# Kernel tuning notes

Hardware: AMD Instinct MI355X
Metric: run time of the kernel (lower is better)

## Reference

```python
import jax, jax.numpy as jnp
from jax import lax
import numpy as np

B, S, R, V, C = 64, 512, 64, 30522, 2


def setup_inputs() -> dict:
    key = jax.random.key(0)
    k1, k2, k3, k4 = jax.random.split(key, 4)
    input_ids = jax.random.randint(k1, (B, S), 0, V, dtype=jnp.int32)
    mask = jnp.ones((B, S), dtype=jnp.int32)
    segment_ids = jnp.zeros((B, S), dtype=jnp.int32)
    seq_lengths = jnp.full((B,), S, dtype=jnp.int32)
    # scale 1/sqrt(R) keeps the 512-step matrix chain numerically stable in fp32
    G_weight = jax.random.normal(k2, (V, R * R), dtype=jnp.float32) * (1.0 / float(np.sqrt(R)))
    G1_weight = jax.random.normal(k3, (R, 1), dtype=jnp.float32) * 0.1
    lin_W = jax.random.normal(k4, (C, R), dtype=jnp.float32) * 0.1
    lin_b = jnp.zeros((C,), dtype=jnp.float32)
    return {"input_ids": input_ids, "mask": mask, "segment_ids": segment_ids,
            "seq_lengths": seq_lengths, "G_weight": G_weight, "G1_weight": G1_weight,
            "lin_W": lin_W, "lin_b": lin_b}


def reference(input_ids, mask, segment_ids, seq_lengths, G_weight, G1_weight, lin_W, lin_b):
    b, s = input_ids.shape
    r = lin_W.shape[1]
    # embedding lookup -> per-token r x r matrices: (b, s, r, r)
    encoded = jnp.take(G_weight, input_ids, axis=0).reshape(b, s, r, r)
    # initial state: G1.weight.view(-1, r) repeated over batch -> (b, 1, r)
    init = jnp.broadcast_to(G1_weight.reshape(1, 1, r), (b, 1, r)).astype(G_weight.dtype)
    # sequential matrix-chain recurrence over sequence positions
    xs = jnp.moveaxis(encoded, 1, 0)  # (s, b, r, r)

    def step(carry, M):
        return jnp.einsum('bij,bjk->bik', carry, M), None

    result, _ = lax.scan(step, init, xs)  # (b, 1, r)
    # torch F.normalize(dim=2): x / max(||x||_2, eps)
    norm = jnp.sqrt(jnp.sum(result * result, axis=2, keepdims=True))
    normed = result / jnp.maximum(norm, 1e-12)
    encoded_x = jnp.squeeze(normed, axis=1)  # (b, r)
    out = encoded_x @ lin_W.T + lin_b  # (b, n_class)
    return jnp.squeeze(out)
```

## Files before the change

kernel.cpp:

```cpp
#include <hip/hip_runtime.h>
#include <math.h>

#define SEQ   512
#define RDIM  64
#define NB    64
#define SEGL  16
#define SEGS  32

typedef short  v4s __attribute__((ext_vector_type(4)));
typedef float  v4f __attribute__((ext_vector_type(4)));
typedef unsigned int u32x2 __attribute__((ext_vector_type(2)));

__device__ __forceinline__ v4f mfma16(v4s a, v4s b, v4f c) {
#if __has_builtin(__builtin_amdgcn_mfma_f32_16x16x16bf16_1k)
    return __builtin_amdgcn_mfma_f32_16x16x16bf16_1k(a, b, c, 0, 0, 0);
#else
    v4f d;
    asm volatile("v_mfma_f32_16x16x16_bf16 %0, %1, %2, %3"
                 : "=v"(d) : "v"(a), "v"(b), "v"(c));
    return d;
#endif
}

__device__ __forceinline__ unsigned short bf16_rne(float x) {
    unsigned int u = __float_as_uint(x);
    unsigned int r = u + 0x7FFFu + ((u >> 16) & 1u);
    return (unsigned short)(r >> 16);
}
__device__ __forceinline__ float bf16_tof(unsigned short h) {
    return __uint_as_float(((unsigned int)h) << 16);
}

__global__ __launch_bounds__(64, 2)
void seg_kernel(const int* __restrict__ input_ids,
                const float* __restrict__ G_weight,
                float* __restrict__ ws)
{
    const int lane = threadIdx.x & 63;
    const int g    = lane >> 4;
    const int rl   = lane & 15;
    const int blk  = blockIdx.x;
    const int idb  = blk << 4;

    v4f acc[4][4];
#pragma unroll
    for (int m = 0; m < 4; ++m)
#pragma unroll
        for (int jb = 0; jb < 4; ++jb)
#pragma unroll
            for (int r = 0; r < 4; ++r)
                acc[m][jb][r] = (m == jb && rl == ((g << 2) + r)) ? 1.0f : 0.0f;

    float4 pa[16];
    {
        const int id0 = __builtin_amdgcn_readfirstlane(input_ids[idb + 15]);
        const float* bp = G_weight + (((size_t)id0) << 12);
#pragma unroll
        for (int m = 0; m < 4; ++m) {
            const float* gp = bp + (((m << 4) + rl) << 6) + (g << 2);
#pragma unroll
            for (int kc = 0; kc < 4; ++kc)
                pa[(m << 2) + kc] = *(const float4*)(gp + (kc << 4));
        }
    }

    int pend = input_ids[idb + 14];

#pragma unroll 1
    for (int i = 0; i < 16; ++i) {
        v4s Bh[4][4], Bl[4][4];
#pragma unroll
        for (int kc = 0; kc < 4; ++kc)
#pragma unroll
            for (int jb = 0; jb < 4; ++jb) {
                v4s h, l;
#pragma unroll
                for (int r = 0; r < 4; ++r) {
                    const float x = acc[kc][jb][r];
                    const unsigned short hh = bf16_rne(x);
                    h[r] = (short)hh;
                    l[r] = (short)bf16_rne(x - bf16_tof(hh));
                }
                Bh[kc][jb] = h;
                Bl[kc][jb] = l;
            }

        const int idn = __builtin_amdgcn_readfirstlane(pend);

#pragma unroll
        for (int m = 0; m < 4; ++m) {
            v4s Ah[4], Al[4];
#pragma unroll
            for (int kc = 0; kc < 4; ++kc) {
                const float4 x = pa[(m << 2) + kc];
                const float e[4] = {x.x, x.y, x.z, x.w};
#pragma unroll
                for (int j = 0; j < 4; ++j) {
                    const unsigned short hh = bf16_rne(e[j]);
                    Ah[kc][j] = (short)hh;
                    Al[kc][j] = (short)bf16_rne(e[j] - bf16_tof(hh));
                }
            }
            if (i < 15) {
                const float* gp = G_weight + (((size_t)idn) << 12)
                                + (((m << 4) + rl) << 6) + (g << 2);
#pragma unroll
                for (int kc = 0; kc < 4; ++kc)
                    pa[(m << 2) + kc] = *(const float4*)(gp + (kc << 4));
            }
#pragma unroll
            for (int jb = 0; jb < 4; ++jb) {
                v4f d = {0.f, 0.f, 0.f, 0.f};
#pragma unroll
                for (int kc = 0; kc < 4; ++kc) {
                    d = mfma16(Ah[kc], Bh[kc][jb], d);
                    d = mfma16(Al[kc], Bh[kc][jb], d);
                    d = mfma16(Ah[kc], Bl[kc][jb], d);
                }
                acc[m][jb] = d;
            }
        }

        {
            int nx = 13 - i;
            nx = (nx < 0) ? 0 : nx;
            pend = input_ids[idb + nx];
        }
    }

    float* wp = ws + (((size_t)blk) << 12);
#pragma unroll
    for (int m = 0; m < 4; ++m)
#pragma unroll
        for (int jb = 0; jb < 4; ++jb)
#pragma unroll
            for (int r = 0; r < 4; ++r)
                wp[(((m << 4) + (g << 2) + r) << 6) + (jb << 4) + rl] = acc[m][jb][r];
}

__device__ __forceinline__ float qreduce4(float x) {
#if __has_builtin(__builtin_amdgcn_permlane16_swap) && __has_builtin(__builtin_amdgcn_permlane32_swap)
    u32x2 a = __builtin_amdgcn_permlane16_swap(__float_as_uint(x), __float_as_uint(x), false, false);
    const float y = __uint_as_float(a.x) + __uint_as_float(a.y);
    u32x2 c = __builtin_amdgcn_permlane32_swap(__float_as_uint(y), __float_as_uint(y), false, false);
    return __uint_as_float(c.x) + __uint_as_float(c.y);
#else
    x += __shfl_xor(x, 16, 64);
    x += __shfl_xor(x, 32, 64);
    return x;
#endif
}

#define STRD 12

__global__ __launch_bounds__(512, 2)
void chain2_kernel(const float* __restrict__ ws,
                   const float* __restrict__ G1_weight,
                   const float* __restrict__ lin_W,
                   const float* __restrict__ lin_b,
                   float* __restrict__ out)
{
    __shared__ __align__(16) float part[2][RDIM][STRD];

    const int tid  = threadIdx.x;
    const int lane = tid & 63;
    const int w    = tid >> 6;
    const int b    = blockIdx.x;
    const int sub  = lane >> 4;
    const int p16  = lane & 15;

    const int k0 = (w << 3) + sub;
    float vm0 = G1_weight[k0];
    float vm1 = G1_weight[k0 + 4];

    const size_t lo0 = (size_t)((w << 9) + (sub << 6) + (p16 << 2));
    const size_t lo1 = lo0 + 256;

    float4 bufA[16], bufB[16];

#define ISSUE2(S, T) do {                                                  \
        const float* bp_ = ws + (((size_t)((b << 5) + (T))) << 12);        \
        bufA[S] = *(const float4*)(bp_ + lo0);                             \
        bufB[S] = *(const float4*)(bp_ + lo1);                             \
    } while (0)

#pragma unroll
    for (int p = 0; p < 16; ++p) ISSUE2(p, p);

#define BODY2(S, T) do {                                                       \
        const float4 a_ = bufA[S];                                             \
        const float4 c_ = bufB[S];                                             \
        float fx = fmaf(vm0, a_.x, vm1 * c_.x);                                \
        float fy = fmaf(vm0, a_.y, vm1 * c_.y);                                \
        float fz = fmaf(vm0, a_.z, vm1 * c_.z);                                \
        float fw = fmaf(vm0, a_.w, vm1 * c_.w);                                \
        { int nx_ = (T) + 16; nx_ = (nx_ < SEGS) ? nx_ : (SEGS - 1);           \
          ISSUE2(S, nx_); }                                                    \
        fx = qreduce4(fx); fy = qreduce4(fy);                                  \
        fz = qreduce4(fz); fw = qreduce4(fw);                                  \
        const float wv_ = (sub == 0) ? fx : (sub == 1) ? fy                    \
                        : (sub == 2) ? fz : fw;                                \
        part[(T) & 1][(p16 << 2) + sub][w] = wv_;                              \
        asm volatile("s_waitcnt lgkmcnt(0)\n\ts_barrier" ::: "memory");        \
        {                                                                      \
            const float4* pk0_ = (const float4*)&part[(T) & 1][k0][0];         \
            const float4  r0_  = pk0_[0], r1_ = pk0_[1];                       \
            vm0 = ((r0_.x + r0_.y) + (r0_.z + r0_.w))                          \
                + ((r1_.x + r1_.y) + (r1_.z + r1_.w));                         \
            const float4* pk1_ = (const float4*)&part[(T) & 1][k0 + 4][0];     \
            const float4  s0_  = pk1_[0], s1_ = pk1_[1];                       \
            vm1 = ((s0_.x + s0_.y) + (s0_.z + s0_.w))                          \
                + ((s1_.x + s1_.y) + (s1_.z + s1_.w));                         \
        }                                                                      \
    } while (0)

    BODY2( 0,  0); BODY2( 1,  1); BODY2( 2,  2); BODY2( 3,  3);
    BODY2( 4,  4); BODY2( 5,  5); BODY2( 6,  6); BODY2( 7,  7);
    BODY2( 8,  8); BODY2( 9,  9); BODY2(10, 10); BODY2(11, 11);
    BODY2(12, 12); BODY2(13, 13); BODY2(14, 14); BODY2(15, 15);
    BODY2( 0, 16); BODY2( 1, 17); BODY2( 2, 18); BODY2( 3, 19);
    BODY2( 4, 20); BODY2( 5, 21); BODY2( 6, 22); BODY2( 7, 23);
    BODY2( 8, 24); BODY2( 9, 25); BODY2(10, 26); BODY2(11, 27);
    BODY2(12, 28); BODY2(13, 29); BODY2(14, 30); BODY2(15, 31);

    asm volatile("s_waitcnt vmcnt(0)" ::: "memory");

    float vj;
    {
        const float4* pj = (const float4*)&part[1][lane][0];
        const float4 q0 = pj[0], q1 = pj[1];
        vj = ((q0.x + q0.y) + (q0.z + q0.w)) + ((q1.x + q1.y) + (q1.z + q1.w));
    }

    if (w == 0) {
        float ss = vj * vj;
#pragma unroll
        for (int off = 32; off >= 1; off >>= 1)
            ss += __shfl_xor(ss, off, 64);
        const float inv = 1.0f / fmaxf(sqrtf(ss), 1e-12f);
        const float nj  = vj * inv;

        float d0 = nj * lin_W[lane];
        float d1 = nj * lin_W[RDIM + lane];
#pragma unroll
        for (int off = 32; off >= 1; off >>= 1) {
            d0 += __shfl_xor(d0, off, 64);
            d1 += __shfl_xor(d1, off, 64);
        }
        if (lane == 0) {
            out[b * 2 + 0] = d0 + lin_b[0];
            out[b * 2 + 1] = d1 + lin_b[1];
        }
    }
}

__global__ __launch_bounds__(512, 2)
void matchain_kernel(const int* __restrict__ input_ids,
                     const float* __restrict__ G_weight,
                     const float* __restrict__ G1_weight,
                     const float* __restrict__ lin_W,
                     const float* __restrict__ lin_b,
                     float* __restrict__ out)
{
    __shared__ int   ids[SEQ];
    __shared__ __align__(16) float part[2][RDIM][STRD];

    const int tid  = threadIdx.x;
    const int lane = tid & 63;
    const int w    = tid >> 6;
    const int b    = blockIdx.x;
    const int sub  = lane >> 4;
    const int p16  = lane & 15;

    ids[tid] = input_ids[b * SEQ + tid];
    __syncthreads();

    const int k0 = (w << 3) + sub;
    float vm0 = G1_weight[k0];
    float vm1 = G1_weight[k0 + 4];

    const size_t lo0 = (size_t)((w << 9) + (sub << 6) + (p16 << 2));
    const size_t lo1 = lo0 + 256;

    float4 bufA[16], bufB[16];

#define ISSUE(S, id_) do {                                        \
        const float* bp_ = G_weight + (((size_t)(id_)) << 12);    \
        bufA[S] = *(const float4*)(bp_ + lo0);                    \
        bufB[S] = *(const float4*)(bp_ + lo1);                    \
    } while (0)

#pragma unroll
    for (int p = 0; p < 16; ++p)
        ISSUE(p, __builtin_amdgcn_readfirstlane(ids[p]));

    int pend = ids[16];

#define BODY(S, K) do {                                                        \
        const float4 a_ = bufA[S];                                             \
        const float4 c_ = bufB[S];                                             \
        float fx = fmaf(vm0, a_.x, vm1 * c_.x);                                \
        float fy = fmaf(vm0, a_.y, vm1 * c_.y);                                \
        float fz = fmaf(vm0, a_.z, vm1 * c_.z);                                \
        float fw = fmaf(vm0, a_.w, vm1 * c_.w);                                \
        {                                                                      \
            const int idn_ = __builtin_amdgcn_readfirstlane(pend);             \
            ISSUE(S, idn_);                                                    \
            int nx_ = t0 + (K) + 17;                                           \
            nx_ = (nx_ < SEQ) ? nx_ : (SEQ - 1);                               \
            pend = ids[nx_];                                                   \
        }                                                                      \
        fx = qreduce4(fx); fy = qreduce4(fy);                                  \
        fz = qreduce4(fz); fw = qreduce4(fw);                                  \
        const float wv_ = (sub == 0) ? fx : (sub == 1) ? fy                    \
                        : (sub == 2) ? fz : fw;                                \
        part[(K) & 1][(p16 << 2) + sub][w] = wv_;                              \
        asm volatile("s_waitcnt lgkmcnt(0)\n\ts_barrier" ::: "memory");        \
        {                                                                      \
            const float4* pk0_ = (const float4*)&part[(K) & 1][k0][0];         \
            const float4  r0_  = pk0_[0], r1_ = pk0_[1];                       \
            vm0 = ((r0_.x + r0_.y) + (r0_.z + r0_.w))                          \
                + ((r1_.x + r1_.y) + (r1_.z + r1_.w));                         \
            const float4* pk1_ = (const float4*)&part[(K) & 1][k0 + 4][0];     \
            const float4  s0_  = pk1_[0], s1_ = pk1_[1];                       \
            vm1 = ((s0_.x + s0_.y) + (s0_.z + s0_.w))                          \
                + ((s1_.x + s1_.y) + (s1_.z + s1_.w));                         \
        }                                                                      \
    } while (0)

#pragma unroll 1
    for (int t0 = 0; t0 < SEQ; t0 += 16) {
        BODY( 0,  0); BODY( 1,  1); BODY( 2,  2); BODY( 3,  3);
        BODY( 4,  4); BODY( 5,  5); BODY( 6,  6); BODY( 7,  7);
        BODY( 8,  8); BODY( 9,  9); BODY(10, 10); BODY(11, 11);
        BODY(12, 12); BODY(13, 13); BODY(14, 14); BODY(15, 15);
    }

    asm volatile("s_waitcnt vmcnt(0)" ::: "memory");

    float vj;
    {
        const float4* pj = (const float4*)&part[1][lane][0];
        const float4 q0 = pj[0], q1 = pj[1];
        vj = ((q0.x + q0.y) + (q0.z + q0.w)) + ((q1.x + q1.y) + (q1.z + q1.w));
    }

    if (w == 0) {
        float ss = vj * vj;
#pragma unroll
        for (int off = 32; off >= 1; off >>= 1)
            ss += __shfl_xor(ss, off, 64);
        const float inv = 1.0f / fmaxf(sqrtf(ss), 1e-12f);
        const float nj  = vj * inv;

        float d0 = nj * lin_W[lane];
        float d1 = nj * lin_W[RDIM + lane];
#pragma unroll
        for (int off = 32; off >= 1; off >>= 1) {
            d0 += __shfl_xor(d0, off, 64);
            d1 += __shfl_xor(d1, off, 64);
        }
        if (lane == 0) {
            out[b * 2 + 0] = d0 + lin_b[0];
            out[b * 2 + 1] = d1 + lin_b[1];
        }
    }
}

extern "C" void kernel_launch(void* const* d_in, const int* in_sizes, int n_in,
                              void* d_out, int out_size, void* d_ws, size_t ws_size,
                              hipStream_t stream) {
    const int*   input_ids = (const int*)d_in[0];
    const float* G_weight  = (const float*)d_in[4];
    const float* G1_weight = (const float*)d_in[5];
    const float* lin_W     = (const float*)d_in[6];
    const float* lin_b     = (const float*)d_in[7];
    float*       out       = (float*)d_out;

    const size_t need = (size_t)NB * SEGS * RDIM * RDIM * sizeof(float);
    if (ws_size >= need) {
        float* ws = (float*)d_ws;
        seg_kernel<<<NB * SEGS, 64, 0, stream>>>(input_ids, G_weight, ws);
        chain2_kernel<<<NB, 512, 0, stream>>>(ws, G1_weight, lin_W, lin_b, out);
    } else {
        matchain_kernel<<<NB, 512, 0, stream>>>(input_ids, G_weight, G1_weight,
                                                lin_W, lin_b, out);
    }
}
```

Baseline: 125.0 us.

## Fuse segment-product and chain kernels with per-batch atomic counters

Merges the segment matrix-product kernel and the chain/output kernel into a single launch. Each 512-thread block runs eight segment waves, then signals a per-batch counter with a release atomic. The first 64 blocks spin until all 32 segments of their batch are done and then run the chain reduction. This removes the second kernel launch and the gap between kernels, but adds a memset, spin-waiting, and a dependence on the first 64 blocks being co-resident with producer blocks to avoid deadlock.

```diff
diff --git a/kernel.cpp b/kernel.cpp
--- a/kernel.cpp
+++ b/kernel.cpp
@@ -4,8 +4,10 @@
 #define SEQ   512
 #define RDIM  64
 #define NB    64
-#define SEGL  16
 #define SEGS  32
+#define NSEG  2048
+#define STRD  12
+#define WS_MATS_BYTES ((size_t)NSEG * RDIM * RDIM * sizeof(float))
 
 typedef short  v4s __attribute__((ext_vector_type(4)));
 typedef float  v4f __attribute__((ext_vector_type(4)));
@@ -29,113 +31,6 @@
 }
 __device__ __forceinline__ float bf16_tof(unsigned short h) {
     return __uint_as_float(((unsigned int)h) << 16);
-}
-
-__global__ __launch_bounds__(64, 2)
-void seg_kernel(const int* __restrict__ input_ids,
-                const float* __restrict__ G_weight,
-                float* __restrict__ ws)
-{
-    const int lane = threadIdx.x & 63;
-    const int g    = lane >> 4;
-    const int rl   = lane & 15;
-    const int blk  = blockIdx.x;
-    const int idb  = blk << 4;
-
-    v4f acc[4][4];
-#pragma unroll
-    for (int m = 0; m < 4; ++m)
-#pragma unroll
-        for (int jb = 0; jb < 4; ++jb)
-#pragma unroll
-            for (int r = 0; r < 4; ++r)
-                acc[m][jb][r] = (m == jb && rl == ((g << 2) + r)) ? 1.0f : 0.0f;
-
-    float4 pa[16];
-    {
-        const int id0 = __builtin_amdgcn_readfirstlane(input_ids[idb + 15]);
-        const float* bp = G_weight + (((size_t)id0) << 12);
-#pragma unroll
-        for (int m = 0; m < 4; ++m) {
-            const float* gp = bp + (((m << 4) + rl) << 6) + (g << 2);
-#pragma unroll
-            for (int kc = 0; kc < 4; ++kc)
-                pa[(m << 2) + kc] = *(const float4*)(gp + (kc << 4));
-        }
-    }
-
-    int pend = input_ids[idb + 14];
-
-#pragma unroll 1
-    for (int i = 0; i < 16; ++i) {
-        v4s Bh[4][4], Bl[4][4];
-#pragma unroll
-        for (int kc = 0; kc < 4; ++kc)
-#pragma unroll
-            for (int jb = 0; jb < 4; ++jb) {
-                v4s h, l;
-#pragma unroll
-                for (int r = 0; r < 4; ++r) {
-                    const float x = acc[kc][jb][r];
-                    const unsigned short hh = bf16_rne(x);
-                    h[r] = (short)hh;
-                    l[r] = (short)bf16_rne(x - bf16_tof(hh));
-                }
-                Bh[kc][jb] = h;
-                Bl[kc][jb] = l;
-            }
-
-        const int idn = __builtin_amdgcn_readfirstlane(pend);
-
-#pragma unroll
-        for (int m = 0; m < 4; ++m) {
-            v4s Ah[4], Al[4];
-#pragma unroll
-            for (int kc = 0; kc < 4; ++kc) {
-                const float4 x = pa[(m << 2) + kc];
-                const float e[4] = {x.x, x.y, x.z, x.w};
-#pragma unroll
-                for (int j = 0; j < 4; ++j) {
-                    const unsigned short hh = bf16_rne(e[j]);
-                    Ah[kc][j] = (short)hh;
-                    Al[kc][j] = (short)bf16_rne(e[j] - bf16_tof(hh));
-                }
-            }
-            if (i < 15) {
-                const float* gp = G_weight + (((size_t)idn) << 12)
-                                + (((m << 4) + rl) << 6) + (g << 2);
-#pragma unroll
-                for (int kc = 0; kc < 4; ++kc)
-                    pa[(m << 2) + kc] = *(const float4*)(gp + (kc << 4));
-            }
-#pragma unroll
-            for (int jb = 0; jb < 4; ++jb) {
-                v4f d = {0.f, 0.f, 0.f, 0.f};
-#pragma unroll
-                for (int kc = 0; kc < 4; ++kc) {
-                    d = mfma16(Ah[kc], Bh[kc][jb], d);
-                    d = mfma16(Al[kc], Bh[kc][jb], d);
-                    d = mfma16(Ah[kc], Bl[kc][jb], d);
-                }
-                acc[m][jb] = d;
-            }
-        }
-
-        {
-            int nx = 13 - i;
-            nx = (nx < 0) ? 0 : nx;
-            pend = input_ids[idb + nx];
-        }
-    }
-
-    float* wp = ws + (((size_t)blk) << 12);
-#pragma unroll
-    for (int m = 0; m < 4; ++m)
-#pragma unroll
-        for (int jb = 0; jb < 4; ++jb)
-#pragma unroll
-            for (int r = 0; r < 4; ++r)
-                wp[(((m << 4) + (g << 2) + r) << 6) + (jb << 4) + rl] = acc[m][jb][r];
 }
 
 __device__ __forceinline__ float qreduce4(float x) {
@@ -151,21 +46,121 @@
 #endif
 }
 
-#define STRD 12
-
-__global__ __launch_bounds__(512, 2)
-void chain2_kernel(const float* __restrict__ ws,
-                   const float* __restrict__ G1_weight,
-                   const float* __restrict__ lin_W,
-                   const float* __restrict__ lin_b,
-                   float* __restrict__ out)
-{
-    __shared__ __align__(16) float part[2][RDIM][STRD];
-
-    const int tid  = threadIdx.x;
+__device__ __forceinline__ void seg_wave(const int* __restrict__ input_ids,
+                                         const float* __restrict__ G_weight,
+                                         float* __restrict__ ws,
+                                         const int seg, const int lane)
+{
+    const int g   = lane >> 4;
+    const int rl  = lane & 15;
+    const int idb = seg << 4;
+
+    v4f acc[4][4];
+#pragma unroll
+    for (int m = 0; m < 4; ++m)
+#pragma unroll
+        for (int jb = 0; jb < 4; ++jb)
+#pragma unroll
+            for (int r = 0; r < 4; ++r)
+                acc[m][jb][r] = (m == jb && rl == ((g << 2) + r)) ? 1.0f : 0.0f;
+
+    float4 pa[16];
+    {
+        const int id0 = __builtin_amdgcn_readfirstlane(input_ids[idb + 15]);
+        const float* bp = G_weight + (((size_t)id0) << 12);
+#pragma unroll
+        for (int m = 0; m < 4; ++m) {
+            const float* gp = bp + (((m << 4) + rl) << 6) + (g << 2);
+#pragma unroll
+            for (int kc = 0; kc < 4; ++kc)
+                pa[(m << 2) + kc] = *(const float4*)(gp + (kc << 4));
+        }
+    }
+
+    int pend = input_ids[idb + 14];
+
+#pragma unroll 1
+    for (int i = 0; i < 16; ++i) {
+        v4s Bh[4][4], Bl[4][4];
+#pragma unroll
+        for (int kc = 0; kc < 4; ++kc)
+#pragma unroll
+            for (int jb = 0; jb < 4; ++jb) {
+                v4s h, l;
+#pragma unroll
+                for (int r = 0; r < 4; ++r) {
+                    const float x = acc[kc][jb][r];
+                    const unsigned short hh = bf16_rne(x);
+                    h[r] = (short)hh;
+                    l[r] = (short)bf16_rne(x - bf16_tof(hh));
+                }
+                Bh[kc][jb] = h;
+                Bl[kc][jb] = l;
+            }
+
+        const int idn = __builtin_amdgcn_readfirstlane(pend);
+
+#pragma unroll
+        for (int m = 0; m < 4; ++m) {
+            v4s Ah[4], Al[4];
+#pragma unroll
+            for (int kc = 0; kc < 4; ++kc) {
+                const float4 x = pa[(m << 2) + kc];
+                const float e[4] = {x.x, x.y, x.z, x.w};
+#pragma unroll
+                for (int j = 0; j < 4; ++j) {
+                    const unsigned short hh = bf16_rne(e[j]);
+                    Ah[kc][j] = (short)hh;
+                    Al[kc][j] = (short)bf16_rne(e[j] - bf16_tof(hh));
+                }
+            }
+            if (i < 15) {
+                const float* gp = G_weight + (((size_t)idn) << 12)
+                                + (((m << 4) + rl) << 6) + (g << 2);
+#pragma unroll
+                for (int kc = 0; kc < 4; ++kc)
+                    pa[(m << 2) + kc] = *(const float4*)(gp + (kc << 4));
+            }
+#pragma unroll
+            for (int jb = 0; jb < 4; ++jb) {
+                v4f d = {0.f, 0.f, 0.f, 0.f};
+#pragma unroll
+                for (int kc = 0; kc < 4; ++kc) {
+                    d = mfma16(Ah[kc], Bh[kc][jb], d);
+                    d = mfma16(Al[kc], Bh[kc][jb], d);
+                    d = mfma16(Ah[kc], Bl[kc][jb], d);
+                }
+                acc[m][jb] = d;
+            }
+        }
+
+        {
+            int nx = 13 - i;
+            nx = (nx < 0) ? 0 : nx;
+            pend = input_ids[idb + nx];
+        }
+    }
+
+    float* wp = ws + (((size_t)seg) << 12);
+#pragma unroll
+    for (int m = 0; m < 4; ++m)
+#pragma unroll
+        for (int jb = 0; jb < 4; ++jb)
+#pragma unroll
+            for (int r = 0; r < 4; ++r)
+                wp[(((m << 4) + (g << 2) + r) << 6) + (jb << 4) + rl] = acc[m][jb][r];
+}
+
+__device__ __forceinline__ void chain_and_out(const float* __restrict__ ws,
+                                              const float* __restrict__ G1_weight,
+                                              const float* __restrict__ lin_W,
+                                              const float* __restrict__ lin_b,
+                                              float* __restrict__ out,
+                                              const int b, const int tid,
+                                              float (*part)[RDIM][STRD])
+{
     const int lane = tid & 63;
     const int w    = tid >> 6;
-    const int b    = blockIdx.x;
     const int sub  = lane >> 4;
     const int p16  = lane & 15;
 
@@ -223,6 +218,9 @@
     BODY2( 8, 24); BODY2( 9, 25); BODY2(10, 26); BODY2(11, 27);
     BODY2(12, 28); BODY2(13, 29); BODY2(14, 30); BODY2(15, 31);
 
+#undef ISSUE2
+#undef BODY2
+
     asm volatile("s_waitcnt vmcnt(0)" ::: "memory");
 
     float vj;
@@ -252,6 +250,61 @@
             out[b * 2 + 1] = d1 + lin_b[1];
         }
     }
+}
+
+__global__ __launch_bounds__(512, 2)
+void fused_kernel(const int* __restrict__ input_ids,
+                  const float* __restrict__ G_weight,
+                  const float* __restrict__ G1_weight,
+                  const float* __restrict__ lin_W,
+                  const float* __restrict__ lin_b,
+                  float* __restrict__ ws,
+                  int* __restrict__ cnt,
+                  float* __restrict__ out)
+{
+    __shared__ __align__(16) float part[2][RDIM][STRD];
+
+    const int tid  = threadIdx.x;
+    const int lane = tid & 63;
+    const int w    = tid >> 6;
+    const int blk  = blockIdx.x;
+    const int seg  = (blk << 3) + w;
+
+    seg_wave(input_ids, G_weight, ws, seg, lane);
+
+    __threadfence();
+    if (lane == 0)
+        __hip_atomic_fetch_add(&cnt[seg >> 5], 1,
+                               __ATOMIC_RELEASE, __HIP_MEMORY_SCOPE_AGENT);
+
+    if (blk < NB) {
+        const int* cp = &cnt[blk];
+        while (__hip_atomic_load(cp, __ATOMIC_ACQUIRE,
+                                 __HIP_MEMORY_SCOPE_AGENT) < SEGS)
+            __builtin_amdgcn_s_sleep(8);
+        __threadfence();
+        __syncthreads();
+        chain_and_out(ws, G1_weight, lin_W, lin_b, out, blk, tid, part);
+    }
+}
+
+__global__ __launch_bounds__(64, 2)
+void seg_kernel(const int* __restrict__ input_ids,
+                const float* __restrict__ G_weight,
+                float* __restrict__ ws)
+{
+    seg_wave(input_ids, G_weight, ws, blockIdx.x, threadIdx.x & 63);
+}
+
+__global__ __launch_bounds__(512, 2)
+void chain2_kernel(const float* __restrict__ ws,
+                   const float* __restrict__ G1_weight,
+                   const float* __restrict__ lin_W,
+                   const float* __restrict__ lin_b,
+                   float* __restrict__ out)
+{
+    __shared__ __align__(16) float part[2][RDIM][STRD];
+    chain_and_out(ws, G1_weight, lin_W, lin_b, out, blockIdx.x, threadIdx.x, part);
 }
 
 __global__ __launch_bounds__(512, 2)
@@ -335,6 +388,8 @@
         BODY( 8,  8); BODY( 9,  9); BODY(10, 10); BODY(11, 11);
         BODY(12, 12); BODY(13, 13); BODY(14, 14); BODY(15, 15);
     }
+#undef ISSUE
+#undef BODY
 
     asm volatile("s_waitcnt vmcnt(0)" ::: "memory");
 
@@ -377,10 +432,16 @@
     const float* lin_b     = (const float*)d_in[7];
     float*       out       = (float*)d_out;
 
-    const size_t need = (size_t)NB * SEGS * RDIM * RDIM * sizeof(float);
-    if (ws_size >= need) {
+    const size_t need_fused = WS_MATS_BYTES + 4096;
+    if (ws_size >= need_fused) {
+        float* ws  = (float*)d_ws;
+        int*   cnt = (int*)((char*)d_ws + WS_MATS_BYTES);
+        hipMemsetAsync(cnt, 0, NB * sizeof(int), stream);
+        fused_kernel<<<NSEG / 8, 512, 0, stream>>>(input_ids, G_weight, G1_weight,
+                                                   lin_W, lin_b, ws, cnt, out);
+    } else if (ws_size >= WS_MATS_BYTES) {
         float* ws = (float*)d_ws;
-        seg_kernel<<<NB * SEGS, 64, 0, stream>>>(input_ids, G_weight, ws);
+        seg_kernel<<<NSEG, 64, 0, stream>>>(input_ids, G_weight, ws);
         chain2_kernel<<<NB, 512, 0, stream>>>(ws, G1_weight, lin_W, lin_b, out);
     } else {
         matchain_kernel<<<NB, 512, 0, stream>>>(input_ids, G_weight, G1_weight,
```

Result: slower. 314.8 us (+151.9%).
